# Optimization experiments

Measured on AMD Instinct MI355X. Metric: run time of the kernel, lower is better.

Reference implementation:

```python
import jax, jax.numpy as jnp
import numpy as np

L, N, E, H, D, F = 2048, 2, 1024, 16, 64, 4096  # seq, batch, embed, heads, head_dim, ffn
EPS = 1e-5


def _ln(x, w, b):
    m = jnp.mean(x, axis=-1, keepdims=True)
    v = jnp.mean(jnp.square(x - m), axis=-1, keepdims=True)
    return (x - m) * jax.lax.rsqrt(v + EPS) * w + b


def setup_inputs() -> dict:
    key = jax.random.key(0)
    ks = jax.random.split(key, 16)
    s = 0.02
    f32 = jnp.float32
    return {
        "x": jax.random.normal(ks[0], (L, N, E), f32),
        "ln1_w": jnp.ones((E,), f32),
        "ln1_b": jnp.zeros((E,), f32),
        "wq": jax.random.normal(ks[1], (H * D, E), f32) * s,
        "bq": jnp.zeros((H * D,), f32),
        "wk": jax.random.normal(ks[2], (H * D, E), f32) * s,
        "bk": jnp.zeros((H * D,), f32),
        "wv": jax.random.normal(ks[3], (H * D, E), f32) * s,
        "bv": jnp.zeros((H * D,), f32),
        "wout": jax.random.normal(ks[4], (E, H * D), f32) * s,
        "bout": jnp.zeros((E,), f32),
        "ln2_w": jnp.ones((E,), f32),
        "ln2_b": jnp.zeros((E,), f32),
        "fc1_w": jax.random.normal(ks[5], (F, E), f32) * s,
        "fc1_b": jnp.zeros((F,), f32),
        "fc2_w": jax.random.normal(ks[6], (E, F), f32) * s,
        "fc2_b": jnp.zeros((E,), f32),
    }


def reference(x, ln1_w, ln1_b, wq, bq, wk, bk, wv, bv, wout, bout,
              ln2_w, ln2_b, fc1_w, fc1_b, fc2_w, fc2_b):
    scale = D ** (-0.5)
    residual = x
    h = _ln(x, ln1_w, ln1_b)                      # (L,N,E)
    q = (h @ wq.T + bq).reshape(L, N, H, D) * scale
    k = (h @ wk.T + bk).reshape(L, N, H, D)
    v = (h @ wv.T + bv).reshape(L, N, H, D)
    attn = jnp.einsum('qnhd,knhd->nhqk', q, k)    # (N,H,L,L) full score matrix
    causal = jnp.tril(jnp.ones((L, L), bool))
    attn = jnp.where(causal[None, None], attn, jnp.float32(-10000.0))
    p = jax.nn.softmax(attn, axis=-1)
    o = jnp.einsum('nhqk,knhd->qnhd', p, v).reshape(L, N, H * D)
    o = o @ wout.T + bout
    x = o + residual
    residual = x
    h = _ln(x, ln2_w, ln2_b)
    h = jax.nn.gelu(h @ fc1_w.T + fc1_b, approximate=False)
    h = h @ fc2_w.T + fc2_b
    return h + residual
```

## Files before the change

kernel.cpp:

```cpp
#include <hip/hip_runtime.h>
#include <hip/hip_bf16.h>
#include <math.h>

using bf16 = __hip_bfloat16;
typedef __bf16 bf16x8 __attribute__((ext_vector_type(8)));
typedef short  short4v __attribute__((ext_vector_type(4)));
typedef float  f32x4  __attribute__((ext_vector_type(4)));

static constexpr int Lq = 2048, Nb = 2, E = 1024, Hh = 16, Dd = 64, Ff = 4096;
static constexpr int MT = Lq * Nb;

__device__ __forceinline__ void async_lds16(const void* g, void* l) {
  __builtin_amdgcn_global_load_lds(
      (const __attribute__((address_space(1))) void*)g,
      (__attribute__((address_space(3))) void*)l, 16, 0, 0);
}
__device__ __forceinline__ bf16x8 ld8(const bf16* p) { return *(const bf16x8*)p; }
__device__ __forceinline__ short bfbits(float x) {
  bf16 t = __float2bfloat16(x);
  return *(short*)&t;
}
__device__ __forceinline__ float gelu_fast(float v) {
  const float y = fminf(2.302208f * (v + 0.044715f * v * v * v), 80.f);
  const float t = exp2f(y);
  return v * t / (t + 1.0f);
}

__global__ __launch_bounds__(256) void cvt_all_kernel(
    const float* __restrict__ wq, const float* __restrict__ wk,
    const float* __restrict__ wv, const float* __restrict__ wout,
    const float* __restrict__ fc1w, const float* __restrict__ fc2w,
    bf16* __restrict__ wqkvb, bf16* __restrict__ woutb,
    bf16* __restrict__ f1wb, bf16* __restrict__ f2wb) {
  const int i = blockIdx.x * 256 + threadIdx.x;
  const float* src;
  bf16* dst;
  size_t off;
  if (i < 786432) {
    const int r = i >> 18;
    off = (size_t)(i & 262143);
    src = (r == 0) ? wq : (r == 1) ? wk : wv;
    dst = wqkvb + (size_t)r * (E * E);
  } else if (i < 1048576) {
    off = (size_t)(i - 786432); src = wout; dst = woutb;
  } else if (i < 2097152) {
    off = (size_t)(i - 1048576); src = fc1w; dst = f1wb;
  } else {
    off = (size_t)(i - 2097152); src = fc2w; dst = f2wb;
  }
  float4 v = ((const float4*)src)[off];
  bf16 o4[4] = {__float2bfloat16(v.x), __float2bfloat16(v.y),
                __float2bfloat16(v.z), __float2bfloat16(v.w)};
  *(uint2*)(dst + 4 * off) = *(uint2*)o4;
}

template <int EPI, int BK>
__global__ __launch_bounds__(256) void gemm_bt(
    const bf16* __restrict__ A, const bf16* __restrict__ W,
    const float* __restrict__ b1, const float* __restrict__ b2,
    const float* __restrict__ b3, int Klen, int Kstride, int Nld,
    float qscale, int scut, bf16* __restrict__ outb,
    bf16* __restrict__ outv, bf16* __restrict__ outk) {
  __shared__ __align__(16) bf16 As[128 * BK];
  __shared__ __align__(16) bf16 Bs[128 * BK];
  const int tid = threadIdx.x;
  const int w = tid >> 6, lane = tid & 63;
  const int quad = lane >> 4, l16 = lane & 15;
  const int wm = (w >> 1) * 64, wn = (w & 1) * 64;
  const int m0 = blockIdx.y * 128, n0 = blockIdx.x * 128;
  const int koff = blockIdx.z * Klen;

  f32x4 acc[4][4];
#pragma unroll
  for (int i = 0; i < 4; i++)
#pragma unroll
    for (int j = 0; j < 4; j++)
#pragma unroll
      for (int r = 0; r < 4; r++) acc[i][j][r] = 0.f;

  if constexpr (BK == 32) {
    const int c0 = w * 64 + lane;
    const int c1 = c0 + 256;
    const size_t arow0 = (size_t)(m0 + (c0 >> 2)), arow1 = (size_t)(m0 + (c1 >> 2));
    const size_t brow0 = (size_t)(n0 + (c0 >> 2)), brow1 = (size_t)(n0 + (c1 >> 2));
    const int col0 = (c0 & 3) * 8, col1 = (c1 & 3) * 8;
    bf16* ldsA0 = &As[(w * 64) * 8];
    bf16* ldsA1 = &As[(256 + w * 64) * 8];
    bf16* ldsB0 = &Bs[(w * 64) * 8];
    bf16* ldsB1 = &Bs[(256 + w * 64) * 8];

    const int nk = Klen >> 5;
    for (int kt = 0; kt < nk; ++kt) {
      const int k0 = koff + kt * 32;
      async_lds16(A + arow0 * Kstride + k0 + col0, ldsA0);
      async_lds16(A + arow1 * Kstride + k0 + col1, ldsA1);
      async_lds16(W + brow0 * Kstride + k0 + col0, ldsB0);
      async_lds16(W + brow1 * Kstride + k0 + col1, ldsB1);
      __syncthreads();
      bf16x8 a[4], b[4];
#pragma unroll
      for (int i = 0; i < 4; i++) {
        a[i] = ld8(&As[(wm + i * 16 + l16) * 32 + quad * 8]);
        b[i] = ld8(&Bs[(wn + i * 16 + l16) * 32 + quad * 8]);
      }
#pragma unroll
      for (int i = 0; i < 4; i++)
#pragma unroll
        for (int j = 0; j < 4; j++)
          acc[i][j] = __builtin_amdgcn_mfma_f32_16x16x32_bf16(a[i], b[j], acc[i][j], 0, 0, 0);
      __syncthreads();
    }
  } else {
    const int rowoff = w * 8 + (lane >> 3);
    const int colsw = (((lane & 7) ^ (lane >> 3)) << 3);

    const int nk = Klen >> 6;
    for (int kt = 0; kt < nk; ++kt) {
      const int k0 = koff + (kt << 6);
#pragma unroll
      for (int r = 0; r < 4; r++) {
        async_lds16(A + (size_t)(m0 + r * 32 + rowoff) * Kstride + k0 + colsw,
                    As + (size_t)(r * 256 + w * 64) * 8);
        async_lds16(W + (size_t)(n0 + r * 32 + rowoff) * Kstride + k0 + colsw,
                    Bs + (size_t)(r * 256 + w * 64) * 8);
      }
      __syncthreads();
#pragma unroll
      for (int ksub = 0; ksub < 2; ksub++) {
        const int gx = ksub * 4 + quad;
        bf16x8 a[4], b[4];
#pragma unroll
        for (int i = 0; i < 4; i++) {
          const int ra = wm + i * 16 + l16;
          const int rb = wn + i * 16 + l16;
          a[i] = ld8(&As[(size_t)(ra * 8 + (gx ^ (l16 & 7))) * 8]);
          b[i] = ld8(&Bs[(size_t)(rb * 8 + (gx ^ (l16 & 7))) * 8]);
        }
#pragma unroll
        for (int i = 0; i < 4; i++)
#pragma unroll
          for (int j = 0; j < 4; j++)
            acc[i][j] = __builtin_amdgcn_mfma_f32_16x16x32_bf16(a[i], b[j], acc[i][j], 0, 0, 0);
      }
      __syncthreads();
    }
  }

  const size_t zoff = (EPI == 3) ? (size_t)blockIdx.z * ((size_t)MT * E) : 0;
#pragma unroll
  for (int i = 0; i < 4; i++) {
    const int mrow = m0 + wm + i * 16 + quad * 4;
#pragma unroll
    for (int j = 0; j < 4; j++) {
      const int ncol = n0 + wn + j * 16 + l16;
      float bv = 0.f;
      if constexpr (EPI != 3) {
        if (b3 != nullptr) {
          bv = (ncol < 1024) ? b1[ncol]
               : (ncol < 2048) ? b2[ncol - 1024] : b3[ncol - 2048];
        } else {
          bv = b1[ncol];
        }
      }
      const float sc = (ncol < scut) ? qscale : 1.0f;
#pragma unroll
      for (int r = 0; r < 4; r++) {
        float v = (acc[i][j][r] + bv) * sc;
        if constexpr (EPI == 2) {
          outb[(size_t)(mrow + r) * Nld + ncol] = __float2bfloat16(gelu_fast(v));
        } else if constexpr (EPI == 3) {
          outb[zoff + (size_t)(mrow + r) * Nld + ncol] = __float2bfloat16(v);
        } else {
          const int tok = mrow + r, n = tok & 1, l = tok >> 1;
          if (ncol < 1024) {
            outb[(size_t)tok * 1024 + ncol] = __float2bfloat16(v);
          } else if (ncol < 2048) {
            const int h = (ncol - 1024) >> 6, d = ncol & 63;
            const int hh = n * 16 + h;
            outk[((((size_t)hh * 32 + (l >> 6)) * 8 + (d >> 3)) * 64 + (l & 63)) * 8 +
                 (d & 7)] = __float2bfloat16(v);
          } else {
            const int h = (ncol - 2048) >> 6, d = ncol & 63;
            const int hh = n * 16 + h;
            outv[((((size_t)hh * 32 + (l >> 6)) * 8 + ((l >> 3) & 7)) * 64 + d) * 8 +
                 (l & 7)] = __float2bfloat16(v);
          }
        }
      }
    }
  }
}

template <int S, int H>
__device__ __forceinline__ void load_frags256(const char* Ab, const char* Bb,
                                              const int (&aoff)[8], const int (&boff)[4],
                                              bf16x8 (&a)[4], bf16x8 (&b)[4]) {
#pragma unroll
  for (int i = 0; i < 4; i++) a[i] = ld8((const bf16*)(Ab + S * 16384 + aoff[H * 4 + i]));
#pragma unroll
  for (int j = 0; j < 4; j++) b[j] = ld8((const bf16*)(Bb + S * 16384 + boff[j]));
}

template <int H>
__device__ __forceinline__ void mfma256(const bf16x8 (&a)[4], const bf16x8 (&b)[4],
                                        f32x4 (&acc)[8][4]) {
#pragma unroll
  for (int i = 0; i < 4; i++)
#pragma unroll
    for (int j = 0; j < 4; j++)
      acc[H * 4 + i][j] =
          __builtin_amdgcn_mfma_f32_16x16x32_bf16(a[i], b[j], acc[H * 4 + i][j], 0, 0, 0);
}

template <int K, int NOUT>
__global__ __launch_bounds__(512, 2) void gemm256_gelu(
    const bf16* __restrict__ A, const bf16* __restrict__ W,
    const float* __restrict__ bias, bf16* __restrict__ out) {
  extern __shared__ char smem[];
  constexpr int NKT = K / 64;
  static_assert(NKT >= 2, "need >=2 K-tiles");
  const int tid = threadIdx.x;
  const int w = tid >> 6, lane = tid & 63;
  const int quad = lane >> 4, l16 = lane & 15;
  const int wr = w >> 2, wc = w & 3;
  const int m0 = blockIdx.y * 256, n0 = blockIdx.x * 256;

  const int o0 = tid << 4;
  const int o1 = o0 + 8192;
  const int r0 = o0 >> 6, r1 = o1 >> 6;
  const int c0 = ((((o0 >> 4) & 3) ^ ((o0 >> 7) & 3)) << 3);
  const int c1 = ((((o1 >> 4) & 3) ^ ((o1 >> 7) & 3)) << 3);
  const bf16* Ag0 = A + (size_t)(m0 + r0) * K + c0;
  const bf16* Ag1 = A + (size_t)(m0 + r1) * K + c1;
  const bf16* Wg0 = W + (size_t)(n0 + r0) * K + c0;
  const bf16* Wg1 = W + (size_t)(n0 + r1) * K + c1;
  const int ldsw = w << 10;

  int aoff[8], boff[4];
#pragma unroll
  for (int h = 0; h < 2; h++)
#pragma unroll
    for (int i = 0; i < 4; i++) {
      const int ra = wr * 128 + h * 64 + i * 16 + l16;
      aoff[h * 4 + i] = ra * 64 + ((quad ^ ((ra >> 1) & 3)) << 4);
    }
#pragma unroll
  for (int j = 0; j < 4; j++) {
    const int rb = wc * 64 + j * 16 + l16;
    boff[j] = rb * 64 + ((quad ^ ((rb >> 1) & 3)) << 4);
  }

  f32x4 acc[8][4];
#pragma unroll
  for (int i = 0; i < 8; i++)
#pragma unroll
    for (int j = 0; j < 4; j++)
#pragma unroll
      for (int r = 0; r < 4; r++) acc[i][j][r] = 0.f;

  {
    char* d = smem;
    async_lds16(Ag0, d + ldsw);
    async_lds16(Ag1, d + 8192 + ldsw);
    async_lds16(Wg0, d + 32768 + ldsw);
    async_lds16(Wg1, d + 32768 + 8192 + ldsw);
    async_lds16(Ag0 + 32, d + 16384 + ldsw);
    async_lds16(Ag1 + 32, d + 16384 + 8192 + ldsw);
    async_lds16(Wg0 + 32, d + 49152 + ldsw);
    async_lds16(Wg1 + 32, d + 49152 + 8192 + ldsw);
  }
  asm volatile("s_waitcnt vmcnt(4)" ::: "memory");
  __builtin_amdgcn_s_barrier();

  for (int kt = 0; kt < NKT; ++kt) {
    const char* Ab = smem + ((kt & 1) << 16);
    const char* Bb = Ab + 32768;
    char* Sd = smem + (((kt + 1) & 1) << 16);
    const int kn = (kt + 1) << 6;
    if (kt + 1 < NKT) {
      {
        bf16x8 a[4], b[4];
        load_frags256<0, 0>(Ab, Bb, aoff, boff, a, b);
        async_lds16(Ag0 + kn, Sd + ldsw);
        async_lds16(Ag1 + kn, Sd + 8192 + ldsw);
        __builtin_amdgcn_s_barrier();
        __builtin_amdgcn_s_setprio(1);
        mfma256<0>(a, b, acc);
        __builtin_amdgcn_s_setprio(0);
        __builtin_amdgcn_sched_barrier(0);
        __builtin_amdgcn_s_barrier();
      }
      {
        bf16x8 a[4], b[4];
        load_frags256<0, 1>(Ab, Bb, aoff, boff, a, b);
        async_lds16(Wg0 + kn, Sd + 32768 + ldsw);
        async_lds16(Wg1 + kn, Sd + 32768 + 8192 + ldsw);
        __builtin_amdgcn_s_barrier();
        __builtin_amdgcn_s_setprio(1);
        mfma256<1>(a, b, acc);
        __builtin_amdgcn_s_setprio(0);
        asm volatile("s_waitcnt vmcnt(4)" ::: "memory");
        __builtin_amdgcn_sched_barrier(0);
        __builtin_amdgcn_s_barrier();
      }
      {
        bf16x8 a[4], b[4];
        load_frags256<1, 0>(Ab, Bb, aoff, boff, a, b);
        async_lds16(Ag0 + kn + 32, Sd + 16384 + ldsw);
        async_lds16(Ag1 + kn + 32, Sd + 16384 + 8192 + ldsw);
        __builtin_amdgcn_s_barrier();
        __builtin_amdgcn_s_setprio(1);
        mfma256<0>(a, b, acc);
        __builtin_amdgcn_s_setprio(0);
        __builtin_amdgcn_sched_barrier(0);
        __builtin_amdgcn_s_barrier();
      }
      {
        bf16x8 a[4], b[4];
        load_frags256<1, 1>(Ab, Bb, aoff, boff, a, b);
        async_lds16(Wg0 + kn + 32, Sd + 49152 + ldsw);
        async_lds16(Wg1 + kn + 32, Sd + 49152 + 8192 + ldsw);
        __builtin_amdgcn_s_barrier();
        __builtin_amdgcn_s_setprio(1);
        mfma256<1>(a, b, acc);
        __builtin_amdgcn_s_setprio(0);
        asm volatile("s_waitcnt vmcnt(4)" ::: "memory");
        __builtin_amdgcn_sched_barrier(0);
        __builtin_amdgcn_s_barrier();
      }
    } else {
      {
        bf16x8 a[4], b[4];
        load_frags256<0, 0>(Ab, Bb, aoff, boff, a, b);
        __builtin_amdgcn_s_barrier();
        __builtin_amdgcn_s_setprio(1);
        mfma256<0>(a, b, acc);
        __builtin_amdgcn_s_setprio(0);
        __builtin_amdgcn_sched_barrier(0);
        __builtin_amdgcn_s_barrier();
      }
      {
        bf16x8 a[4], b[4];
        load_frags256<0, 1>(Ab, Bb, aoff, boff, a, b);
        __builtin_amdgcn_s_barrier();
        __builtin_amdgcn_s_setprio(1);
        mfma256<1>(a, b, acc);
        __builtin_amdgcn_s_setprio(0);
        asm volatile("s_waitcnt vmcnt(0)" ::: "memory");
        __builtin_amdgcn_sched_barrier(0);
        __builtin_amdgcn_s_barrier();
      }
      {
        bf16x8 a[4], b[4];
        load_frags256<1, 0>(Ab, Bb, aoff, boff, a, b);
        __builtin_amdgcn_s_barrier();
        __builtin_amdgcn_s_setprio(1);
        mfma256<0>(a, b, acc);
        __builtin_amdgcn_s_setprio(0);
        __builtin_amdgcn_sched_barrier(0);
        __builtin_amdgcn_s_barrier();
      }
      {
        bf16x8 a[4], b[4];
        load_frags256<1, 1>(Ab, Bb, aoff, boff, a, b);
        __builtin_amdgcn_s_barrier();
        __builtin_amdgcn_s_setprio(1);
        mfma256<1>(a, b, acc);
        __builtin_amdgcn_s_setprio(0);
      }
    }
  }

#pragma unroll
  for (int j = 0; j < 4; j++) {
    const int col = n0 + wc * 64 + j * 16 + l16;
    const float bv = bias[col];
#pragma unroll
    for (int mI = 0; mI < 8; mI++) {
      const int row = m0 + wr * 128 + mI * 16 + quad * 4;
#pragma unroll
      for (int r = 0; r < 4; r++) {
        out[(size_t)(row + r) * NOUT + col] =
            __float2bfloat16(gelu_fast(acc[mI][j][r] + bv));
      }
    }
  }
}

__global__ __launch_bounds__(256) void reduce2_kernel(
    const bf16* __restrict__ P, const float* __restrict__ bias,
    const float* __restrict__ res, float* __restrict__ out) {
  const int i = blockIdx.x * 256 + threadIdx.x;
  const size_t e0 = (size_t)i * 4;
  const int col = (int)(e0 & (E - 1));
  uint2 u0 = *(const uint2*)(P + e0);
  uint2 u1 = *(const uint2*)(P + (size_t)MT * E + e0);
  const bf16* p0 = (const bf16*)&u0;
  const bf16* p1 = (const bf16*)&u1;
  float4 b = *(const float4*)(bias + col);
  float4 r = *(const float4*)(res + e0);
  float4 o;
  o.x = (float)p0[0] + (float)p1[0] + b.x + r.x;
  o.y = (float)p0[1] + (float)p1[1] + b.y + r.y;
  o.z = (float)p0[2] + (float)p1[2] + b.z + r.z;
  o.w = (float)p0[3] + (float)p1[3] + b.w + r.w;
  *(float4*)(out + e0) = o;
}

__global__ __launch_bounds__(256) void redln_kernel(
    const bf16* __restrict__ P, const float* __restrict__ bias,
    const float* __restrict__ res, const float* __restrict__ wgt,
    const float* __restrict__ bia, float* __restrict__ x1,
    bf16* __restrict__ h2) {
  const int t = blockIdx.x, tid = threadIdx.x;
  const size_t base = (size_t)t * E;
  const int e0 = tid * 4;
  uint2 u0 = *(const uint2*)(P + base + e0);
  uint2 u1 = *(const uint2*)(P + (size_t)MT * E + base + e0);
  const bf16* p0 = (const bf16*)&u0;
  const bf16* p1 = (const bf16*)&u1;
  float4 b = *(const float4*)(bias + e0);
  float4 r = *(const float4*)(res + base + e0);
  float v4[4];
  v4[0] = (float)p0[0] + (float)p1[0] + b.x + r.x;
  v4[1] = (float)p0[1] + (float)p1[1] + b.y + r.y;
  v4[2] = (float)p0[2] + (float)p1[2] + b.z + r.z;
  v4[3] = (float)p0[3] + (float)p1[3] + b.w + r.w;
  *(float4*)(x1 + base + e0) = *(float4*)v4;

  float s = 0.f, ss = 0.f;
#pragma unroll
  for (int i = 0; i < 4; i++) { s += v4[i]; ss += v4[i] * v4[i]; }
  for (int off = 32; off > 0; off >>= 1) {
    s += __shfl_down(s, off, 64);
    ss += __shfl_down(ss, off, 64);
  }
  __shared__ float rs[4], rss[4], mv[2];
  const int w = tid >> 6;
  if ((tid & 63) == 0) { rs[w] = s; rss[w] = ss; }
  __syncthreads();
  if (tid == 0) {
    float S = rs[0] + rs[1] + rs[2] + rs[3];
    float SS = rss[0] + rss[1] + rss[2] + rss[3];
    float mean = S * (1.f / E);
    float var = SS * (1.f / E) - mean * mean;
    mv[0] = mean; mv[1] = rsqrtf(var + 1e-5f);
  }
  __syncthreads();
  const float mean = mv[0], rstd = mv[1];
  float4 wg = *(const float4*)(wgt + e0);
  float4 bb = *(const float4*)(bia + e0);
  bf16 o4[4];
  o4[0] = __float2bfloat16((v4[0] - mean) * rstd * wg.x + bb.x);
  o4[1] = __float2bfloat16((v4[1] - mean) * rstd * wg.y + bb.y);
  o4[2] = __float2bfloat16((v4[2] - mean) * rstd * wg.z + bb.z);
  o4[3] = __float2bfloat16((v4[3] - mean) * rstd * wg.w + bb.w);
  *(uint2*)(h2 + base + e0) = *(uint2*)o4;
}

__global__ __launch_bounds__(256) void ln_kernel(
    const float* __restrict__ x, const float* __restrict__ wgt,
    const float* __restrict__ bia, bf16* __restrict__ out) {
  const int t = blockIdx.x, tid = threadIdx.x;
  const size_t base = (size_t)t * E;
  float v4[4], s = 0.f, ss = 0.f;
#pragma unroll
  for (int i = 0; i < 4; i++) {
    float v = x[base + i * 256 + tid];
    v4[i] = v; s += v; ss += v * v;
  }
  for (int off = 32; off > 0; off >>= 1) {
    s += __shfl_down(s, off, 64);
    ss += __shfl_down(ss, off, 64);
  }
  __shared__ float rs[4], rss[4], mv[2];
  const int w = tid >> 6;
  if ((tid & 63) == 0) { rs[w] = s; rss[w] = ss; }
  __syncthreads();
  if (tid == 0) {
    float S = rs[0] + rs[1] + rs[2] + rs[3];
    float SS = rss[0] + rss[1] + rss[2] + rss[3];
    float mean = S * (1.f / E);
    float var = SS * (1.f / E) - mean * mean;
    mv[0] = mean; mv[1] = rsqrtf(var + 1e-5f);
  }
  __syncthreads();
  const float mean = mv[0], rstd = mv[1];
#pragma unroll
  for (int i = 0; i < 4; i++) {
    const int e = i * 256 + tid;
    float r = (v4[i] - mean) * rstd * wgt[e] + bia[e];
    out[base + e] = __float2bfloat16(r);
  }
}

__global__ __launch_bounds__(256) void attn_kernel(
    const bf16* __restrict__ Q1, const bf16* __restrict__ KT,
    const bf16* __restrict__ VT, bf16* __restrict__ O) {
  __shared__ __align__(16) bf16 KB[2][512 * 8];
  __shared__ __align__(16) bf16 VB[2][512 * 8];
  const int tid = threadIdx.x;
  const int w = tid >> 6, lane = tid & 63, quad = lane >> 4, l16 = lane & 15;
  const int bid = blockIdx.x;
  const int x = bid & 7;
  const int m = (bid >> 3) & 31;
  const int g = bid >> 8;
  const int j = m >> 2;
  const int hh = (m & 3) * 8 + x;
  const int qt = (g == 0) ? j : (g == 1) ? (31 - j) : (g == 2) ? (j + 8) : (23 - j);
  const int n = hh >> 4, h = hh & 15;

  const bf16* Qp = Q1 + n * E + h * Dd;
  const bf16* Kb = KT + (size_t)hh * 32 * 4096;
  const bf16* Vb = VT + (size_t)hh * 32 * 4096;
  const int so = w * 512 + lane * 8;

  const int ql = qt * 64 + w * 16 + l16;
  const bf16x8 aq0 = ld8(Qp + (size_t)ql * 2048 + quad * 8);
  const bf16x8 aq1 = ld8(Qp + (size_t)ql * 2048 + 32 + quad * 8);
  asm volatile("s_waitcnt vmcnt(0)" ::: "memory");

  async_lds16(Kb + so, &KB[0][w * 512]);
  async_lds16(Kb + 2048 + so, &KB[0][2048 + w * 512]);
  async_lds16(Vb + so, &VB[0][w * 512]);
  async_lds16(Vb + 2048 + so, &VB[0][2048 + w * 512]);

  f32x4 o_acc[4];
#pragma unroll
  for (int d = 0; d < 4; d++)
#pragma unroll
    for (int r = 0; r < 4; r++) o_acc[d][r] = 0.f;
  float m_run = -3e30f, l_run = 0.f;

  for (int kt = 0; kt <= qt; ++kt) {
    const bf16* KBb = KB[kt & 1];
    const bf16* VBb = VB[kt & 1];
    if (kt < qt) {
      const size_t tb = (size_t)(kt + 1) * 4096;
      bf16* Kd = &KB[(kt & 1) ^ 1][0];
      bf16* Vd = &VB[(kt & 1) ^ 1][0];
      async_lds16(Kb + tb + so, Kd + w * 512);
      async_lds16(Kb + tb + 2048 + so, Kd + 2048 + w * 512);
      async_lds16(Vb + tb + so, Vd + w * 512);
      async_lds16(Vb + tb + 2048 + so, Vd + 2048 + w * 512);
      asm volatile("s_waitcnt vmcnt(4)" ::: "memory");
    } else {
      asm volatile("s_waitcnt vmcnt(0)" ::: "memory");
    }
    __builtin_amdgcn_s_barrier();

    f32x4 s[4];
    __builtin_amdgcn_s_setprio(1);
#pragma unroll
    for (int ks = 0; ks < 4; ks++) {
      const bf16x8 kc0 = ld8(&KBb[(size_t)((quad)*64 + ks * 16 + l16) * 8]);
      const bf16x8 kc1 = ld8(&KBb[(size_t)((4 + quad) * 64 + ks * 16 + l16) * 8]);
#pragma unroll
      for (int r = 0; r < 4; r++) s[ks][r] = 0.f;
      s[ks] = __builtin_amdgcn_mfma_f32_16x16x32_bf16(kc0, aq0, s[ks], 0, 0, 0);
      s[ks] = __builtin_amdgcn_mfma_f32_16x16x32_bf16(kc1, aq1, s[ks], 0, 0, 0);
    }
    __builtin_amdgcn_s_setprio(0);

    if (kt == qt) {
#pragma unroll
      for (int ks = 0; ks < 4; ks++) {
#pragma unroll
        for (int r = 0; r < 4; r++) {
          const int kg = kt * 64 + ks * 16 + quad * 4 + r;
          if (kg > ql) s[ks][r] = -14427.0f;
        }
      }
    }

    float tmax = s[0][0];
#pragma unroll
    for (int ks = 0; ks < 4; ks++)
#pragma unroll
      for (int r = 0; r < 4; r++) tmax = fmaxf(tmax, s[ks][r]);
    tmax = fmaxf(tmax, __shfl_xor(tmax, 16, 64));
    tmax = fmaxf(tmax, __shfl_xor(tmax, 32, 64));
    float mbase = m_run;
    if (__any(tmax - m_run > 8.0f)) {
      const float mnew = fmaxf(m_run, tmax);
      const float alpha = exp2f(m_run - mnew);
      m_run = mnew;
      mbase = mnew;
      l_run *= alpha;
#pragma unroll
      for (int d = 0; d < 4; d++)
#pragma unroll
        for (int r = 0; r < 4; r++) o_acc[d][r] *= alpha;
    }
    float rsum = 0.f;
    short4v pf[4];
#pragma unroll
    for (int ks = 0; ks < 4; ks++) {
#pragma unroll
      for (int r = 0; r < 4; r++) {
        const float pv = exp2f(s[ks][r] - mbase);
        rsum += pv;
        pf[ks][r] = bfbits(pv);
      }
    }
    rsum += __shfl_xor(rsum, 16, 64);
    rsum += __shfl_xor(rsum, 32, 64);
    l_run += rsum;

    __builtin_amdgcn_s_setprio(1);
#pragma unroll
    for (int d = 0; d < 4; d++) {
#pragma unroll
      for (int ks = 0; ks < 4; ks++) {
        const int gg = ks * 2 + (quad >> 1);
        const short4v av =
            *(const short4v*)&VBb[(size_t)(gg * 64 + d * 16 + l16) * 8 + (quad & 1) * 4];
        o_acc[d] = __builtin_amdgcn_mfma_f32_16x16x16bf16_1k(av, pf[ks], o_acc[d], 0, 0, 0);
      }
    }
    __builtin_amdgcn_s_setprio(0);

    __builtin_amdgcn_sched_barrier(0);
    __builtin_amdgcn_s_barrier();
  }

  const float inv_l = 1.f / fmaxf(l_run, 1e-30f);
  const size_t obase = (size_t)ql * (Nb * E) + (size_t)n * E + h * Dd;
#pragma unroll
  for (int d = 0; d < 4; d++)
#pragma unroll
    for (int r = 0; r < 4; r++)
      O[obase + d * 16 + quad * 4 + r] = __float2bfloat16(o_acc[d][r] * inv_l);
}

extern "C" void kernel_launch(void* const* d_in, const int* in_sizes, int n_in,
                              void* d_out, int out_size, void* d_ws, size_t ws_size,
                              hipStream_t stream) {
  const float* x    = (const float*)d_in[0];
  const float* ln1w = (const float*)d_in[1];
  const float* ln1b = (const float*)d_in[2];
  const float* wq   = (const float*)d_in[3];
  const float* bq   = (const float*)d_in[4];
  const float* wk   = (const float*)d_in[5];
  const float* bk   = (const float*)d_in[6];
  const float* wv   = (const float*)d_in[7];
  const float* bv   = (const float*)d_in[8];
  const float* wout = (const float*)d_in[9];
  const float* bout = (const float*)d_in[10];
  const float* ln2w = (const float*)d_in[11];
  const float* ln2b = (const float*)d_in[12];
  const float* fc1w = (const float*)d_in[13];
  const float* fc1b = (const float*)d_in[14];
  const float* fc2w = (const float*)d_in[15];
  const float* fc2b = (const float*)d_in[16];

  char* ws = (char*)d_ws;
  bf16* wqkvb = (bf16*)(ws);
  bf16* woutb = (bf16*)(ws + ((size_t)6 << 20));
  bf16* f1wb  = (bf16*)(ws + ((size_t)8 << 20));
  bf16* f2wb  = (bf16*)(ws + ((size_t)16 << 20));
  bf16* h1    = (bf16*)(ws + ((size_t)24 << 20));
  bf16* qk1   = (bf16*)(ws + ((size_t)32 << 20));
  bf16* ktg   = (bf16*)(ws + ((size_t)40 << 20));
  bf16* vtg   = (bf16*)(ws + ((size_t)48 << 20));
  bf16* o     = (bf16*)(ws + ((size_t)56 << 20));
  float* x1   = (float*)(ws + ((size_t)64 << 20));
  bf16* Pout  = (bf16*)(ws + ((size_t)32 << 20));
  bf16* P01   = (bf16*)(ws);
  bf16* f1    = (bf16*)(ws + ((size_t)32 << 20));
  bf16* h2    = h1;
  float* outp = (float*)d_out;

  static bool g_shmem_attr = false;
  if (!g_shmem_attr) {
    hipFuncSetAttribute(reinterpret_cast<const void*>(gemm256_gelu<1024, 4096>),
                        hipFuncAttributeMaxDynamicSharedMemorySize, 131072);
    g_shmem_attr = true;
  }

  cvt_all_kernel<<<12288, 256, 0, stream>>>(wq, wk, wv, wout, fc1w, fc2w,
                                            wqkvb, woutb, f1wb, f2wb);

  ln_kernel<<<MT, 256, 0, stream>>>(x, ln1w, ln1b, h1);

  dim3 gQKV(3 * E / 128, MT / 128);
  dim3 gE2(E / 128, MT / 128, 2);

  gemm_bt<4, 64><<<gQKV, 256, 0, stream>>>(h1, wqkvb, bq, bk, bv, E, E, 2048,
                                           0.125f * 1.44269504f, 1024, qk1, vtg, ktg);

  attn_kernel<<<1024, 256, 0, stream>>>(qk1, ktg, vtg, o);

  gemm_bt<3, 64><<<gE2, 256, 0, stream>>>(o, woutb, nullptr, nullptr, nullptr,
                                          E / 2, E, E, 1.f, 0, Pout, nullptr, nullptr);
  redln_kernel<<<MT, 256, 0, stream>>>(Pout, bout, x, ln2w, ln2b, x1, h2);

  gemm256_gelu<1024, 4096><<<dim3(Ff / 256, MT / 256), 512, 131072, stream>>>(
      h2, f1wb, fc1b, f1);

  gemm_bt<3, 64><<<gE2, 256, 0, stream>>>(f1, f2wb, nullptr, nullptr, nullptr,
                                          Ff / 2, Ff, E, 1.f, 0, P01, nullptr, nullptr);
  reduce2_kernel<<<MT * E / 1024, 256, 0, stream>>>(P01, fc2b, x1, outp);
}
```

Baseline: 371.5 us.

## Route QKV, out-proj and FC2 GEMMs through the pipelined 256x256 kernel

Generalizes the 256x256 software-pipelined GEMM used for FC1 with a K-stride, split-K offset and per-use epilogues (QKV scatter, split-K partials, GELU). The 128x128 gemm_bt kernel is removed. The QKV, out-projection (split-K 2) and FC2 (split-K 4) GEMMs now run on the larger tile to get more data reuse per block. The post-attention residual goes straight into the output buffer, and a 4-way reduce kernel folds the FC2 partials together with the bias and residual. The cost is far fewer blocks for the smaller GEMMs (128–256 on a large GPU), which may leave CUs idle, plus extra partial traffic for split-K 4.

```diff
diff --git a/kernel.cpp b/kernel.cpp
--- a/kernel.cpp
+++ b/kernel.cpp
@@ -54,143 +54,6 @@
   *(uint2*)(dst + 4 * off) = *(uint2*)o4;
 }
 
-template <int EPI, int BK>
-__global__ __launch_bounds__(256) void gemm_bt(
-    const bf16* __restrict__ A, const bf16* __restrict__ W,
-    const float* __restrict__ b1, const float* __restrict__ b2,
-    const float* __restrict__ b3, int Klen, int Kstride, int Nld,
-    float qscale, int scut, bf16* __restrict__ outb,
-    bf16* __restrict__ outv, bf16* __restrict__ outk) {
-  __shared__ __align__(16) bf16 As[128 * BK];
-  __shared__ __align__(16) bf16 Bs[128 * BK];
-  const int tid = threadIdx.x;
-  const int w = tid >> 6, lane = tid & 63;
-  const int quad = lane >> 4, l16 = lane & 15;
-  const int wm = (w >> 1) * 64, wn = (w & 1) * 64;
-  const int m0 = blockIdx.y * 128, n0 = blockIdx.x * 128;
-  const int koff = blockIdx.z * Klen;
-
-  f32x4 acc[4][4];
-#pragma unroll
-  for (int i = 0; i < 4; i++)
-#pragma unroll
-    for (int j = 0; j < 4; j++)
-#pragma unroll
-      for (int r = 0; r < 4; r++) acc[i][j][r] = 0.f;
-
-  if constexpr (BK == 32) {
-    const int c0 = w * 64 + lane;
-    const int c1 = c0 + 256;
-    const size_t arow0 = (size_t)(m0 + (c0 >> 2)), arow1 = (size_t)(m0 + (c1 >> 2));
-    const size_t brow0 = (size_t)(n0 + (c0 >> 2)), brow1 = (size_t)(n0 + (c1 >> 2));
-    const int col0 = (c0 & 3) * 8, col1 = (c1 & 3) * 8;
-    bf16* ldsA0 = &As[(w * 64) * 8];
-    bf16* ldsA1 = &As[(256 + w * 64) * 8];
-    bf16* ldsB0 = &Bs[(w * 64) * 8];
-    bf16* ldsB1 = &Bs[(256 + w * 64) * 8];
-
-    const int nk = Klen >> 5;
-    for (int kt = 0; kt < nk; ++kt) {
-      const int k0 = koff + kt * 32;
-      async_lds16(A + arow0 * Kstride + k0 + col0, ldsA0);
-      async_lds16(A + arow1 * Kstride + k0 + col1, ldsA1);
-      async_lds16(W + brow0 * Kstride + k0 + col0, ldsB0);
-      async_lds16(W + brow1 * Kstride + k0 + col1, ldsB1);
-      __syncthreads();
-      bf16x8 a[4], b[4];
-#pragma unroll
-      for (int i = 0; i < 4; i++) {
-        a[i] = ld8(&As[(wm + i * 16 + l16) * 32 + quad * 8]);
-        b[i] = ld8(&Bs[(wn + i * 16 + l16) * 32 + quad * 8]);
-      }
-#pragma unroll
-      for (int i = 0; i < 4; i++)
-#pragma unroll
-        for (int j = 0; j < 4; j++)
-          acc[i][j] = __builtin_amdgcn_mfma_f32_16x16x32_bf16(a[i], b[j], acc[i][j], 0, 0, 0);
-      __syncthreads();
-    }
-  } else {
-    const int rowoff = w * 8 + (lane >> 3);
-    const int colsw = (((lane & 7) ^ (lane >> 3)) << 3);
-
-    const int nk = Klen >> 6;
-    for (int kt = 0; kt < nk; ++kt) {
-      const int k0 = koff + (kt << 6);
-#pragma unroll
-      for (int r = 0; r < 4; r++) {
-        async_lds16(A + (size_t)(m0 + r * 32 + rowoff) * Kstride + k0 + colsw,
-                    As + (size_t)(r * 256 + w * 64) * 8);
-        async_lds16(W + (size_t)(n0 + r * 32 + rowoff) * Kstride + k0 + colsw,
-                    Bs + (size_t)(r * 256 + w * 64) * 8);
-      }
-      __syncthreads();
-#pragma unroll
-      for (int ksub = 0; ksub < 2; ksub++) {
-        const int gx = ksub * 4 + quad;
-        bf16x8 a[4], b[4];
-#pragma unroll
-        for (int i = 0; i < 4; i++) {
-          const int ra = wm + i * 16 + l16;
-          const int rb = wn + i * 16 + l16;
-          a[i] = ld8(&As[(size_t)(ra * 8 + (gx ^ (l16 & 7))) * 8]);
-          b[i] = ld8(&Bs[(size_t)(rb * 8 + (gx ^ (l16 & 7))) * 8]);
-        }
-#pragma unroll
-        for (int i = 0; i < 4; i++)
-#pragma unroll
-          for (int j = 0; j < 4; j++)
-            acc[i][j] = __builtin_amdgcn_mfma_f32_16x16x32_bf16(a[i], b[j], acc[i][j], 0, 0, 0);
-      }
-      __syncthreads();
-    }
-  }
-
-  const size_t zoff = (EPI == 3) ? (size_t)blockIdx.z * ((size_t)MT * E) : 0;
-#pragma unroll
-  for (int i = 0; i < 4; i++) {
-    const int mrow = m0 + wm + i * 16 + quad * 4;
-#pragma unroll
-    for (int j = 0; j < 4; j++) {
-      const int ncol = n0 + wn + j * 16 + l16;
-      float bv = 0.f;
-      if constexpr (EPI != 3) {
-        if (b3 != nullptr) {
-          bv = (ncol < 1024) ? b1[ncol]
-               : (ncol < 2048) ? b2[ncol - 1024] : b3[ncol - 2048];
-        } else {
-          bv = b1[ncol];
-        }
-      }
-      const float sc = (ncol < scut) ? qscale : 1.0f;
-#pragma unroll
-      for (int r = 0; r < 4; r++) {
-        float v = (acc[i][j][r] + bv) * sc;
-        if constexpr (EPI == 2) {
-          outb[(size_t)(mrow + r) * Nld + ncol] = __float2bfloat16(gelu_fast(v));
-        } else if constexpr (EPI == 3) {
-          outb[zoff + (size_t)(mrow + r) * Nld + ncol] = __float2bfloat16(v);
-        } else {
-          const int tok = mrow + r, n = tok & 1, l = tok >> 1;
-          if (ncol < 1024) {
-            outb[(size_t)tok * 1024 + ncol] = __float2bfloat16(v);
-          } else if (ncol < 2048) {
-            const int h = (ncol - 1024) >> 6, d = ncol & 63;
-            const int hh = n * 16 + h;
-            outk[((((size_t)hh * 32 + (l >> 6)) * 8 + (d >> 3)) * 64 + (l & 63)) * 8 +
-                 (d & 7)] = __float2bfloat16(v);
-          } else {
-            const int h = (ncol - 2048) >> 6, d = ncol & 63;
-            const int hh = n * 16 + h;
-            outv[((((size_t)hh * 32 + (l >> 6)) * 8 + ((l >> 3) & 7)) * 64 + d) * 8 +
-                 (l & 7)] = __float2bfloat16(v);
-          }
-        }
-      }
-    }
-  }
-}
-
 template <int S, int H>
 __device__ __forceinline__ void load_frags256(const char* Ab, const char* Bb,
                                               const int (&aoff)[8], const int (&boff)[4],
@@ -212,10 +75,13 @@
           __builtin_amdgcn_mfma_f32_16x16x32_bf16(a[i], b[j], acc[H * 4 + i][j], 0, 0, 0);
 }
 
-template <int K, int NOUT>
-__global__ __launch_bounds__(512, 2) void gemm256_gelu(
+template <int K, int KSTR, int NOUT, int EPI>
+__global__ __launch_bounds__(512, 2) void gemm256(
     const bf16* __restrict__ A, const bf16* __restrict__ W,
-    const float* __restrict__ bias, bf16* __restrict__ out) {
+    const float* __restrict__ b1, const float* __restrict__ b2,
+    const float* __restrict__ b3, float qscale,
+    bf16* __restrict__ o0, bf16* __restrict__ o1,
+    bf16* __restrict__ o2, bf16* __restrict__ o3) {
   extern __shared__ char smem[];
   constexpr int NKT = K / 64;
   static_assert(NKT >= 2, "need >=2 K-tiles");
@@ -224,16 +90,17 @@
   const int quad = lane >> 4, l16 = lane & 15;
   const int wr = w >> 2, wc = w & 3;
   const int m0 = blockIdx.y * 256, n0 = blockIdx.x * 256;
-
-  const int o0 = tid << 4;
-  const int o1 = o0 + 8192;
-  const int r0 = o0 >> 6, r1 = o1 >> 6;
-  const int c0 = ((((o0 >> 4) & 3) ^ ((o0 >> 7) & 3)) << 3);
-  const int c1 = ((((o1 >> 4) & 3) ^ ((o1 >> 7) & 3)) << 3);
-  const bf16* Ag0 = A + (size_t)(m0 + r0) * K + c0;
-  const bf16* Ag1 = A + (size_t)(m0 + r1) * K + c1;
-  const bf16* Wg0 = W + (size_t)(n0 + r0) * K + c0;
-  const bf16* Wg1 = W + (size_t)(n0 + r1) * K + c1;
+  const int koff = blockIdx.z * K;
+
+  const int o0b = tid << 4;
+  const int o1b = o0b + 8192;
+  const int r0 = o0b >> 6, r1 = o1b >> 6;
+  const int c0 = ((((o0b >> 4) & 3) ^ ((o0b >> 7) & 3)) << 3);
+  const int c1 = ((((o1b >> 4) & 3) ^ ((o1b >> 7) & 3)) << 3);
+  const bf16* Ag0 = A + (size_t)(m0 + r0) * KSTR + koff + c0;
+  const bf16* Ag1 = A + (size_t)(m0 + r1) * KSTR + koff + c1;
+  const bf16* Wg0 = W + (size_t)(n0 + r0) * KSTR + koff + c0;
+  const bf16* Wg1 = W + (size_t)(n0 + r1) * KSTR + koff + c1;
   const int ldsw = w << 10;
 
   int aoff[8], boff[4];
@@ -371,46 +238,98 @@
     }
   }
 
-#pragma unroll
-  for (int j = 0; j < 4; j++) {
-    const int col = n0 + wc * 64 + j * 16 + l16;
-    const float bv = bias[col];
-#pragma unroll
-    for (int mI = 0; mI < 8; mI++) {
-      const int row = m0 + wr * 128 + mI * 16 + quad * 4;
-#pragma unroll
-      for (int r = 0; r < 4; r++) {
-        out[(size_t)(row + r) * NOUT + col] =
-            __float2bfloat16(gelu_fast(acc[mI][j][r] + bv));
-      }
-    }
-  }
-}
-
-__global__ __launch_bounds__(256) void reduce2_kernel(
-    const bf16* __restrict__ P, const float* __restrict__ bias,
-    const float* __restrict__ res, float* __restrict__ out) {
+  if constexpr (EPI == 2) {
+#pragma unroll
+    for (int j = 0; j < 4; j++) {
+      const int col = n0 + wc * 64 + j * 16 + l16;
+      const float bv = b1[col];
+#pragma unroll
+      for (int mI = 0; mI < 8; mI++) {
+        const int row = m0 + wr * 128 + mI * 16 + quad * 4;
+#pragma unroll
+        for (int r = 0; r < 4; r++) {
+          o0[(size_t)(row + r) * NOUT + col] =
+              __float2bfloat16(gelu_fast(acc[mI][j][r] + bv));
+        }
+      }
+    }
+  } else if constexpr (EPI == 3) {
+    bf16* dst = (blockIdx.z == 0) ? o0
+              : (blockIdx.z == 1) ? o1
+              : (blockIdx.z == 2) ? o2 : o3;
+#pragma unroll
+    for (int j = 0; j < 4; j++) {
+      const int col = n0 + wc * 64 + j * 16 + l16;
+#pragma unroll
+      for (int mI = 0; mI < 8; mI++) {
+        const int row = m0 + wr * 128 + mI * 16 + quad * 4;
+#pragma unroll
+        for (int r = 0; r < 4; r++) {
+          dst[(size_t)(row + r) * NOUT + col] = __float2bfloat16(acc[mI][j][r]);
+        }
+      }
+    }
+  } else {
+    const int seg = n0 >> 10;
+#pragma unroll
+    for (int j = 0; j < 4; j++) {
+      const int col = n0 + wc * 64 + j * 16 + l16;
+      const float bv = (seg == 0) ? b1[col]
+                     : (seg == 1) ? b2[col - 1024] : b3[col - 2048];
+      const int d = col & 63;
+#pragma unroll
+      for (int mI = 0; mI < 8; mI++) {
+        const int row = m0 + wr * 128 + mI * 16 + quad * 4;
+#pragma unroll
+        for (int r = 0; r < 4; r++) {
+          const int tok = row + r, n = tok & 1, l = tok >> 1;
+          float v = acc[mI][j][r] + bv;
+          if (seg == 0) {
+            o0[(size_t)tok * 1024 + col] = __float2bfloat16(v * qscale);
+          } else if (seg == 1) {
+            const int h = (col - 1024) >> 6, hh = n * 16 + h;
+            o2[((((size_t)hh * 32 + (l >> 6)) * 8 + (d >> 3)) * 64 + (l & 63)) * 8 +
+               (d & 7)] = __float2bfloat16(v);
+          } else {
+            const int h = (col - 2048) >> 6, hh = n * 16 + h;
+            o1[((((size_t)hh * 32 + (l >> 6)) * 8 + ((l >> 3) & 7)) * 64 + d) * 8 +
+               (l & 7)] = __float2bfloat16(v);
+          }
+        }
+      }
+    }
+  }
+}
+
+__global__ __launch_bounds__(256) void reduce4_kernel(
+    const bf16* __restrict__ P0, const bf16* __restrict__ P1,
+    const bf16* __restrict__ P2, const bf16* __restrict__ P3,
+    const float* __restrict__ bias, float* __restrict__ out) {
   const int i = blockIdx.x * 256 + threadIdx.x;
   const size_t e0 = (size_t)i * 4;
   const int col = (int)(e0 & (E - 1));
-  uint2 u0 = *(const uint2*)(P + e0);
-  uint2 u1 = *(const uint2*)(P + (size_t)MT * E + e0);
-  const bf16* p0 = (const bf16*)&u0;
-  const bf16* p1 = (const bf16*)&u1;
+  uint2 a0 = *(const uint2*)(P0 + e0);
+  uint2 a1 = *(const uint2*)(P1 + e0);
+  uint2 a2 = *(const uint2*)(P2 + e0);
+  uint2 a3 = *(const uint2*)(P3 + e0);
+  const bf16* q0 = (const bf16*)&a0;
+  const bf16* q1 = (const bf16*)&a1;
+  const bf16* q2 = (const bf16*)&a2;
+  const bf16* q3 = (const bf16*)&a3;
   float4 b = *(const float4*)(bias + col);
-  float4 r = *(const float4*)(res + e0);
+  float4 r = *(const float4*)(out + e0);
   float4 o;
-  o.x = (float)p0[0] + (float)p1[0] + b.x + r.x;
-  o.y = (float)p0[1] + (float)p1[1] + b.y + r.y;
-  o.z = (float)p0[2] + (float)p1[2] + b.z + r.z;
-  o.w = (float)p0[3] + (float)p1[3] + b.w + r.w;
+  o.x = (float)q0[0] + (float)q1[0] + (float)q2[0] + (float)q3[0] + b.x + r.x;
+  o.y = (float)q0[1] + (float)q1[1] + (float)q2[1] + (float)q3[1] + b.y + r.y;
+  o.z = (float)q0[2] + (float)q1[2] + (float)q2[2] + (float)q3[2] + b.z + r.z;
+  o.w = (float)q0[3] + (float)q1[3] + (float)q2[3] + (float)q3[3] + b.w + r.w;
   *(float4*)(out + e0) = o;
 }
 
 __global__ __launch_bounds__(256) void redln_kernel(
     const bf16* __restrict__ P, const float* __restrict__ bias,
     const float* __restrict__ res, const float* __restrict__ wgt,
-    const float* __restrict__ bia, float* __restrict__ x1,
+    const float* __restrict__ bia, float* __restrict__ resout,
     bf16* __restrict__ h2) {
   const int t = blockIdx.x, tid = threadIdx.x;
   const size_t base = (size_t)t * E;
@@ -426,7 +345,7 @@
   v4[1] = (float)p0[1] + (float)p1[1] + b.y + r.y;
   v4[2] = (float)p0[2] + (float)p1[2] + b.z + r.z;
   v4[3] = (float)p0[3] + (float)p1[3] + b.w + r.w;
-  *(float4*)(x1 + base + e0) = *(float4*)v4;
+  *(float4*)(resout + base + e0) = *(float4*)v4;
 
   float s = 0.f, ss = 0.f;
 #pragma unroll
@@ -664,16 +583,24 @@
   bf16* ktg   = (bf16*)(ws + ((size_t)40 << 20));
   bf16* vtg   = (bf16*)(ws + ((size_t)48 << 20));
   bf16* o     = (bf16*)(ws + ((size_t)56 << 20));
-  float* x1   = (float*)(ws + ((size_t)64 << 20));
   bf16* Pout  = (bf16*)(ws + ((size_t)32 << 20));
-  bf16* P01   = (bf16*)(ws);
   bf16* f1    = (bf16*)(ws + ((size_t)32 << 20));
   bf16* h2    = h1;
+  bf16* FP0   = (bf16*)(ws);
+  bf16* FP1   = (bf16*)(ws + ((size_t)8 << 20));
+  bf16* FP2   = (bf16*)(ws + ((size_t)64 << 20));
+  bf16* FP3   = (bf16*)(ws + ((size_t)72 << 20));
   float* outp = (float*)d_out;
 
   static bool g_shmem_attr = false;
   if (!g_shmem_attr) {
-    hipFuncSetAttribute(reinterpret_cast<const void*>(gemm256_gelu<1024, 4096>),
+    hipFuncSetAttribute(reinterpret_cast<const void*>(gemm256<1024, 1024, 3072, 4>),
+                        hipFuncAttributeMaxDynamicSharedMemorySize, 131072);
+    hipFuncSetAttribute(reinterpret_cast<const void*>(gemm256<512, 1024, 1024, 3>),
+                        hipFuncAttributeMaxDynamicSharedMemorySize, 131072);
+    hipFuncSetAttribute(reinterpret_cast<const void*>(gemm256<1024, 1024, 4096, 2>),
+                        hipFuncAttributeMaxDynamicSharedMemorySize, 131072);
+    hipFuncSetAttribute(reinterpret_cast<const void*>(gemm256<1024, 4096, 1024, 3>),
                         hipFuncAttributeMaxDynamicSharedMemorySize, 131072);
     g_shmem_attr = true;
   }
@@ -683,22 +610,20 @@
 
   ln_kernel<<<MT, 256, 0, stream>>>(x, ln1w, ln1b, h1);
 
-  dim3 gQKV(3 * E / 128, MT / 128);
-  dim3 gE2(E / 128, MT / 128, 2);
-
-  gemm_bt<4, 64><<<gQKV, 256, 0, stream>>>(h1, wqkvb, bq, bk, bv, E, E, 2048,
-                                           0.125f * 1.44269504f, 1024, qk1, vtg, ktg);
+  gemm256<1024, 1024, 3072, 4><<<dim3(12, 16), 512, 131072, stream>>>(
+      h1, wqkvb, bq, bk, bv, 0.125f * 1.44269504f, qk1, vtg, ktg, nullptr);
 
   attn_kernel<<<1024, 256, 0, stream>>>(qk1, ktg, vtg, o);
 
-  gemm_bt<3, 64><<<gE2, 256, 0, stream>>>(o, woutb, nullptr, nullptr, nullptr,
-                                          E / 2, E, E, 1.f, 0, Pout, nullptr, nullptr);
-  redln_kernel<<<MT, 256, 0, stream>>>(Pout, bout, x, ln2w, ln2b, x1, h2);
-
-  gemm256_gelu<1024, 4096><<<dim3(Ff / 256, MT / 256), 512, 131072, stream>>>(
-      h2, f1wb, fc1b, f1);
-
-  gemm_bt<3, 64><<<gE2, 256, 0, stream>>>(f1, f2wb, nullptr, nullptr, nullptr,
-                                          Ff / 2, Ff, E, 1.f, 0, P01, nullptr, nullptr);
-  reduce2_kernel<<<MT * E / 1024, 256, 0, stream>>>(P01, fc2b, x1, outp);
-}
+  gemm256<512, 1024, 1024, 3><<<dim3(4, 16, 2), 512, 131072, stream>>>(
+      o, woutb, nullptr, nullptr, nullptr, 1.f,
+      Pout, Pout + (size_t)MT * E, nullptr, nullptr);
+  redln_kernel<<<MT, 256, 0, stream>>>(Pout, bout, x, ln2w, ln2b, outp, h2);
+
+  gemm256<1024, 1024, 4096, 2><<<dim3(Ff / 256, MT / 256), 512, 131072, stream>>>(
+      h2, f1wb, fc1b, nullptr, nullptr, 1.f, f1, nullptr, nullptr, nullptr);
+
+  gemm256<1024, 4096, 1024, 3><<<dim3(4, 16, 4), 512, 131072, stream>>>(
+      f1, f2wb, nullptr, nullptr, nullptr, 1.f, FP0, FP1, FP2, FP3);
+  reduce4_kernel<<<MT * E / 1024, 256, 0, stream>>>(FP0, FP1, FP2, FP3, fc2b, outp);
+}
```

Result: no change. 367.4 us (-1.1%).
